# Kernel optimization log

Measured on AMD Instinct MI355X. Metric: run time of the kernel, lower is better.

Reference implementation:

```python
import jax, jax.numpy as jnp
import numpy as np

N = 1024          # nodes per atom and per input graph / barycenter
K = 8             # num_atoms
OT_LAYERS = 3     # proximal-point outer iterations inside fgwd
SINKHORN_LAYERS = 3
GWB_LAYERS = 2    # barycenter alternating-optimization iterations
PROX_BETA = 0.1   # proximal / entropic regularization strength
EPS = 1e-16


def fgwd(Gs, ps, Gb, pb):
    """Gromov-Wasserstein distance via proximal point + Sinkhorn.
    Gs:(ns,ns), ps:(ns,1), Gb:(nb,nb), pb:(nb,1). Returns (d, T) with T:(ns,nb).
    Square-loss GW cost: c(T) = f1(Gs) ps 1^T + 1 (f2(Gb) pb)^T - 2 Gs T Gb^T."""
    ns, nb = Gs.shape[0], Gb.shape[0]
    cost_st = ((Gs * Gs) @ ps) + ((Gb * Gb) @ pb).T  # (ns,1)+(1,nb) -> (ns,nb)
    T0 = ps @ pb.T  # independent-coupling init

    def ot_step(T, _):
        cost = cost_st - 2.0 * (Gs @ T @ Gb.T)
        kernel = jnp.exp(-cost / PROX_BETA) * T  # proximal-point kernel

        def sink(carry, _):
            a, b = carry
            b = pb / (kernel.T @ a + EPS)
            a = ps / (kernel @ b + EPS)
            return (a, b), None

        (a, b), _ = jax.lax.scan(sink, (ps, pb), None, length=SINKHORN_LAYERS)
        return (a * kernel) * b.T, None

    T, _ = jax.lax.scan(ot_step, T0, None, length=OT_LAYERS)
    cost = cost_st - 2.0 * (Gs @ T @ Gb.T)
    d = jnp.sum(cost * T)
    return d, T


def setup_inputs() -> dict:
    key = jax.random.key(0)
    k1, k2, k3 = jax.random.split(key, 3)
    Gm = jax.random.uniform(k1, (N, N), jnp.float32)          # input graph (sigmoid-range adjacency)
    pm = jnp.ones((N, 1), jnp.float32) / N                    # uniform node distribution
    atoms_presig = jax.random.normal(k2, (K, N, N), jnp.float32)  # pre-sigmoid atom params
    probs = jnp.ones((K, N, 1), jnp.float32) / N              # uniform atom distributions
    weights = jax.nn.softmax(jax.random.normal(k3, (K,), jnp.float32))  # output_weights
    return {"Gm": Gm, "pm": pm, "atoms_presig": atoms_presig, "probs": probs,
            "weights": weights}


def reference(Gm, pm, atoms_presig, probs, weights):
    Gk = jax.nn.sigmoid(atoms_presig)              # output_atoms: (K,N,N)
    G_bary, pb = Gm, pm                            # init_mode=0 -> barycenter init from input M
    fgwd_v = jax.vmap(fgwd, in_axes=(0, 0, None, None))
    denom = pb @ pb.T                              # pb pb^T normalizer
    for _ in range(GWB_LAYERS):
        _, trans = fgwd_v(Gk, probs, G_bary, pb)   # trans: (K,N,N)
        # comp_fgwb: sum_k w_k * T_k^T G_k T_k / (pb pb^T)
        GT = jnp.einsum('knm,kmj->knj', Gk, trans)
        G_bary = jnp.einsum('k,kni,knj->ij', weights, trans, GT) / denom
    d_fgw, _ = fgwd(Gm, pm, G_bary, pb)
    return d_fgw, G_bary
```

## Files before the change

kernel.cpp:

```cpp
#include <hip/hip_runtime.h>
#include <math.h>

#define N_   1024
#define K_   8
#define OTL  3
#define SKL  3
#define GWBL 2
#define INVB 10.0f
#define EPSV 1e-16f
#define INVN (1.0f / 1024.0f)
#define NN   ((size_t)N_ * N_)
#define KN   (K_ * N_)

typedef __attribute__((ext_vector_type(8))) short short8;
typedef __attribute__((ext_vector_type(4))) float f32x4;
typedef unsigned short bfu;

__device__ __forceinline__ float b2f(bfu u) {
    unsigned x = ((unsigned)u) << 16;
    return __builtin_bit_cast(float, x);
}
__device__ __forceinline__ bfu f2b(float f) {
    unsigned u = __builtin_bit_cast(unsigned, f);
    unsigned r = u + 0x7fffu + ((u >> 16) & 1u);
    return (bfu)(r >> 16);
}

template<int EPI>
__global__ __launch_bounds__(256, 2)
void bgemm_k(const bfu* __restrict__ A, const bfu* __restrict__ B,
             void* __restrict__ Cp, size_t sA, size_t sB, size_t sC,
             const float* __restrict__ rv, const float* __restrict__ cv,
             const float* __restrict__ wts, float* __restrict__ rs) {
    __shared__ bfu As[128 * 32];
    __shared__ bfu Bs[128 * 32];

    const int z  = blockIdx.x;
    const int bm = blockIdx.y * 128, bn = blockIdx.z * 128;
    const int tid = threadIdx.x;
    const int lane = tid & 63, wv = tid >> 6;
    const int wr = wv >> 1, wc = wv & 1;

    if (EPI == 0) {
        if (rs && blockIdx.y == 0 && blockIdx.z == 0) {
            const float4 zf = {0.f, 0.f, 0.f, 0.f};
            #pragma unroll
            for (int b = 0; b < 3; ++b)
                *(float4*)&rs[b * KN + z * N_ + tid * 4] = zf;
        }
    }

    const bfu* Az = A + (size_t)z * sA;
    const bfu* Bz = B + (size_t)z * sB;

    const int sr = tid >> 2;
    const int sk = (tid & 3) * 8;
    const int fr = lane & 15;
    const int ks = (lane >> 4) * 8;

    f32x4 acc[4][4];
    #pragma unroll
    for (int i = 0; i < 4; i++)
        #pragma unroll
        for (int j = 0; j < 4; j++) acc[i][j] = (f32x4)0.f;

    for (int k0 = 0; k0 < N_; k0 += 32) {
        __syncthreads();
        #pragma unroll
        for (int h = 0; h < 2; ++h) {
            const int row = sr + h * 64;
            const bfu* ga = Az + (size_t)(bm + row) * N_ + k0 + sk;
            const bfu* gb = Bz + (size_t)(bn + row) * N_ + k0 + sk;
            __builtin_amdgcn_global_load_lds(
                (const __attribute__((address_space(1))) unsigned int*)ga,
                (__attribute__((address_space(3))) unsigned int*)&As[row * 32 + sk],
                16, 0, 0);
            __builtin_amdgcn_global_load_lds(
                (const __attribute__((address_space(1))) unsigned int*)gb,
                (__attribute__((address_space(3))) unsigned int*)&Bs[row * 32 + sk],
                16, 0, 0);
        }
        __syncthreads();

        short8 af[4], bf[4];
        #pragma unroll
        for (int mi = 0; mi < 4; ++mi)
            af[mi] = *(const short8*)&As[(wr * 64 + mi * 16 + fr) * 32 + ks];
        #pragma unroll
        for (int ni = 0; ni < 4; ++ni)
            bf[ni] = *(const short8*)&Bs[(wc * 64 + ni * 16 + fr) * 32 + ks];
        #pragma unroll
        for (int mi = 0; mi < 4; ++mi)
            #pragma unroll
            for (int ni = 0; ni < 4; ++ni)
                acc[mi][ni] = __builtin_amdgcn_mfma_f32_16x16x32_bf16(
                    af[mi], bf[ni], acc[mi][ni], 0, 0, 0);
    }

    const int r0 = bm + wr * 64, c0 = bn + wc * 64;
    const int rq = (lane >> 4) * 4;

    if (EPI == 1) {
        float* Cz = (float*)Cp + (size_t)z * sC;
        const float w = wts[z];
        #pragma unroll
        for (int mi = 0; mi < 4; ++mi)
            #pragma unroll
            for (int ni = 0; ni < 4; ++ni)
                #pragma unroll
                for (int q = 0; q < 4; ++q)
                    Cz[(size_t)(r0 + mi * 16 + rq + q) * N_ + c0 + ni * 16 + fr]
                        = w * acc[mi][ni][q];
    } else if (EPI == 0) {
        bfu* Cz = (bfu*)Cp + (size_t)z * sC;
        #pragma unroll
        for (int mi = 0; mi < 4; ++mi)
            #pragma unroll
            for (int ni = 0; ni < 4; ++ni)
                #pragma unroll
                for (int q = 0; q < 4; ++q)
                    Cz[(size_t)(r0 + mi * 16 + rq + q) * N_ + c0 + ni * 16 + fr]
                        = f2b(acc[mi][ni][q]);
    } else {
        bfu* Cz = (bfu*)Cp + (size_t)z * sC;
        const float* rvz = rv + z * N_;
        float rsum[4][4];
        #pragma unroll
        for (int mi = 0; mi < 4; ++mi)
            #pragma unroll
            for (int q = 0; q < 4; ++q) rsum[mi][q] = 0.f;
        #pragma unroll
        for (int mi = 0; mi < 4; ++mi)
            #pragma unroll
            for (int ni = 0; ni < 4; ++ni)
                #pragma unroll
                for (int q = 0; q < 4; ++q) {
                    const int row = r0 + mi * 16 + rq + q;
                    const int col = c0 + ni * 16 + fr;
                    const float cost = rvz[col] + cv[row] - 2.f * acc[mi][ni][q];
                    const float t = b2f(Cz[(size_t)row * N_ + col]);
                    const bfu tn = f2b(expf(-cost * INVB) * t);
                    Cz[(size_t)row * N_ + col] = tn;
                    rsum[mi][q] += b2f(tn);
                }
        #pragma unroll
        for (int mi = 0; mi < 4; ++mi)
            #pragma unroll
            for (int q = 0; q < 4; ++q) {
                float v = rsum[mi][q];
                v += __shfl_xor(v, 1);
                v += __shfl_xor(v, 2);
                v += __shfl_xor(v, 4);
                v += __shfl_xor(v, 8);
                if (fr == 0)
                    atomicAdd(&rs[z * N_ + r0 + mi * 16 + rq + q], v);
            }
    }
}

template<int EPI>
__global__ __launch_bounds__(256, 2)
void gemm64_k(const bfu* __restrict__ A, const bfu* __restrict__ B,
              void* __restrict__ Cp,
              const float* __restrict__ rv, const float* __restrict__ cv,
              float* __restrict__ rs, float* __restrict__ dout) {
    __shared__ bfu As[64 * 32];
    __shared__ bfu Bs[64 * 32];
    const int bn = blockIdx.x * 64;
    const int bm = blockIdx.y * 64;
    const int tid = threadIdx.x;
    const int lane = tid & 63, wv = tid >> 6;
    const int wr = wv >> 1, wc = wv & 1;
    const int sr = tid >> 2, sk = (tid & 3) * 8;
    const int fr = lane & 15, ks = (lane >> 4) * 8;

    if (EPI == 0) {
        if (blockIdx.x == 0 && blockIdx.y == 0) {
            if (rs) {
                const float4 zf = {0.f, 0.f, 0.f, 0.f};
                #pragma unroll
                for (int b = 0; b < 3; ++b)
                    *(float4*)&rs[b * KN + tid * 4] = zf;
            }
            if (dout && tid == 0) *dout = 0.f;
        }
    }

    f32x4 acc[2][2];
    #pragma unroll
    for (int i = 0; i < 2; i++)
        #pragma unroll
        for (int j = 0; j < 2; j++) acc[i][j] = (f32x4)0.f;

    for (int k0 = 0; k0 < N_; k0 += 32) {
        __syncthreads();
        __builtin_amdgcn_global_load_lds(
            (const __attribute__((address_space(1))) unsigned int*)
                (A + (size_t)(bm + sr) * N_ + k0 + sk),
            (__attribute__((address_space(3))) unsigned int*)&As[sr * 32 + sk],
            16, 0, 0);
        __builtin_amdgcn_global_load_lds(
            (const __attribute__((address_space(1))) unsigned int*)
                (B + (size_t)(bn + sr) * N_ + k0 + sk),
            (__attribute__((address_space(3))) unsigned int*)&Bs[sr * 32 + sk],
            16, 0, 0);
        __syncthreads();
        short8 af[2], bf[2];
        #pragma unroll
        for (int mi = 0; mi < 2; ++mi)
            af[mi] = *(const short8*)&As[(wr * 32 + mi * 16 + fr) * 32 + ks];
        #pragma unroll
        for (int ni = 0; ni < 2; ++ni)
            bf[ni] = *(const short8*)&Bs[(wc * 32 + ni * 16 + fr) * 32 + ks];
        #pragma unroll
        for (int mi = 0; mi < 2; ++mi)
            #pragma unroll
            for (int ni = 0; ni < 2; ++ni)
                acc[mi][ni] = __builtin_amdgcn_mfma_f32_16x16x32_bf16(
                    af[mi], bf[ni], acc[mi][ni], 0, 0, 0);
    }

    const int r0 = bm + wr * 32, c0 = bn + wc * 32;
    const int rq = (lane >> 4) * 4;

    if (EPI == 0) {
        bfu* C = (bfu*)Cp;
        #pragma unroll
        for (int mi = 0; mi < 2; ++mi)
            #pragma unroll
            for (int ni = 0; ni < 2; ++ni)
                #pragma unroll
                for (int q = 0; q < 4; ++q)
                    C[(size_t)(r0 + mi * 16 + rq + q) * N_ + c0 + ni * 16 + fr]
                        = f2b(acc[mi][ni][q]);
    } else if (EPI == 2) {
        bfu* C = (bfu*)Cp;
        float rsum[2][4];
        #pragma unroll
        for (int mi = 0; mi < 2; ++mi)
            #pragma unroll
            for (int q = 0; q < 4; ++q) rsum[mi][q] = 0.f;
        #pragma unroll
        for (int mi = 0; mi < 2; ++mi)
            #pragma unroll
            for (int ni = 0; ni < 2; ++ni)
                #pragma unroll
                for (int q = 0; q < 4; ++q) {
                    const int row = r0 + mi * 16 + rq + q;
                    const int col = c0 + ni * 16 + fr;
                    const float cost = rv[col] + cv[row] - 2.f * acc[mi][ni][q];
                    const float t = b2f(C[(size_t)row * N_ + col]);
                    const bfu tn = f2b(expf(-cost * INVB) * t);
                    C[(size_t)row * N_ + col] = tn;
                    rsum[mi][q] += b2f(tn);
                }
        #pragma unroll
        for (int mi = 0; mi < 2; ++mi)
            #pragma unroll
            for (int q = 0; q < 4; ++q) {
                float v = rsum[mi][q];
                v += __shfl_xor(v, 1);
                v += __shfl_xor(v, 2);
                v += __shfl_xor(v, 4);
                v += __shfl_xor(v, 8);
                if (fr == 0)
                    atomicAdd(&rs[r0 + mi * 16 + rq + q], v);
            }
    } else {
        const bfu* C = (const bfu*)Cp;
        float bs = 0.f;
        #pragma unroll
        for (int mi = 0; mi < 2; ++mi)
            #pragma unroll
            for (int ni = 0; ni < 2; ++ni)
                #pragma unroll
                for (int q = 0; q < 4; ++q) {
                    const int row = r0 + mi * 16 + rq + q;
                    const int col = c0 + ni * 16 + fr;
                    bs += (rv[col] + cv[row] - 2.f * acc[mi][ni][q]) *
                          b2f(C[(size_t)row * N_ + col]);
                }
        #pragma unroll
        for (int off = 32; off; off >>= 1) bs += __shfl_down(bs, off);
        __shared__ float wred[4];
        if (lane == 0) wred[wv] = bs;
        __syncthreads();
        if (tid == 0) atomicAdd(dout, wred[0] + wred[1] + wred[2] + wred[3]);
    }
}

__global__ __launch_bounds__(256)
void prox1_k(bfu* __restrict__ Tt, const float* __restrict__ c2,
             const float* __restrict__ u, const float* __restrict__ d2,
             const float* __restrict__ w, const float* __restrict__ ps,
             const float* __restrict__ pb, float* __restrict__ bv,
             float* __restrict__ rs1, int zs, int nb) {
    const int b = blockIdx.x;
    const int z  = (nb == 8) ? (b & 7) : 0;
    const int rp = (nb == 8) ? (b >> 3) : b;
    const int tid = threadIdx.x;

    if (rp < 2) {
        const float4 zf = {0.f, 0.f, 0.f, 0.f};
        *(float4*)&rs1[rp * KN + z * N_ + tid * 4] = zf;
    }

    const int half = tid >> 7;
    const int j = rp * 2 + half;
    const int i0 = (tid & 127) * 8;
    const float d2j = d2[j], wj = w[j], pbj = pb[j];
    const float* c2z = c2 + z * zs + i0;
    const float* uz  = u  + z * zs + i0;
    const float* psz = ps + z * zs + i0;
    bfu o[8];
    float s = 0.f;
    #pragma unroll
    for (int t = 0; t < 8; ++t) {
        const float cost = c2z[t] + d2j - 2.f * uz[t] * wj;
        o[t] = f2b(expf(-cost * INVB) * psz[t] * pbj);
        s += b2f(o[t]);
    }
    *(short8*)&Tt[((size_t)z << 20) + ((size_t)j << 10) + i0] = *(short8*)o;
    #pragma unroll
    for (int off = 32; off; off >>= 1) s += __shfl_down(s, off);
    __shared__ float red[4];
    if ((tid & 63) == 0) red[tid >> 6] = s;
    __syncthreads();
    if ((tid & 127) == 0)
        bv[z * N_ + j] = pbj / ((red[half * 2] + red[half * 2 + 1]) * INVN + EPSV);
}

template<int NB, int BSRC, int TUPD>
__global__ __launch_bounds__(1024)
void sinka_k(bfu* __restrict__ Tt, const float* __restrict__ bvin,
             const float* __restrict__ rsin, const float* __restrict__ ps,
             int pstr, float* __restrict__ rsnext) {
    constexpr int CPB = (NB == 8) ? 32 : 16;
    constexpr int RG  = 1024 / CPB;
    constexpr int RPG = N_ / RG;
    int z, cb;
    if (NB == 8) { z = blockIdx.x & 7; cb = blockIdx.x >> 3; }
    else         { z = 0;              cb = blockIdx.x; }
    const int tid = threadIdx.x;
    const int cl = tid % CPB, rg = tid / CPB;
    const int i = cb * CPB + cl;
    const int zN = z * N_;
    bfu* Tz = Tt + (size_t)z * NN;

    __shared__ float bvs[1024];
    __shared__ float red[1024];
    __shared__ float avs[CPB];
    if (BSRC == 0)      bvs[tid] = bvin[zN + tid];
    else if (BSRC == 1) bvs[tid] = INVN / (rsin[zN + tid] * INVN + EPSV);
    else                bvs[tid] = INVN / (rsin[zN + tid] + EPSV);
    __syncthreads();

    float s = 0.f;
    const int j0 = rg * RPG;
    #pragma unroll 8
    for (int j = j0; j < j0 + RPG; ++j)
        s += b2f(Tz[(size_t)j * N_ + i]) * bvs[j];
    red[tid] = s;
    __syncthreads();
    #pragma unroll
    for (int h = RG / 2; h > 0; h >>= 1) {
        if (rg < h) red[rg * CPB + cl] += red[(rg + h) * CPB + cl];
        __syncthreads();
    }
    const float avi = ps[z * pstr + i] / (red[cl] + EPSV);

    if (TUPD) {
        for (int j = j0; j < j0 + RPG; ++j) {
            const size_t o = (size_t)j * N_ + i;
            Tz[o] = f2b(b2f(Tz[o]) * avi * bvs[j]);
        }
    } else {
        if (rg == 0) avs[cl] = avi;
        __syncthreads();
        const bfu* Tr = Tz + (size_t)tid * N_ + cb * CPB;
        float v = 0.f;
        #pragma unroll
        for (int q8 = 0; q8 < CPB; q8 += 8) {
            bfu t[8];
            *(short8*)t = *(const short8*)&Tr[q8];
            #pragma unroll
            for (int q = 0; q < 8; ++q) v += b2f(t[q]) * avs[q8 + q];
        }
        atomicAdd(&rsnext[zN + tid], v);
    }
}


template<int SIG>
__global__ void prep_k(const float* __restrict__ X, bfu* __restrict__ Y,
                       float* __restrict__ y2, float* __restrict__ y1) {
    const int z = blockIdx.y;
    const int wv = threadIdx.x >> 6, lane = threadIdx.x & 63;
    const int r = blockIdx.x * 4 + wv;
    const float* Xr = X + (size_t)z * NN + (size_t)r * N_;
    bfu* Yr = Y + (size_t)z * NN + (size_t)r * N_;
    float s2 = 0.f, s1 = 0.f;
    for (int c = lane * 4; c < N_; c += 256) {
        float4 v = *(const float4*)(Xr + c);
        if (SIG) {
            v.x = 1.f / (1.f + expf(-v.x));
            v.y = 1.f / (1.f + expf(-v.y));
            v.z = 1.f / (1.f + expf(-v.z));
            v.w = 1.f / (1.f + expf(-v.w));
        }
        bfu o[4];
        o[0] = f2b(v.x); o[1] = f2b(v.y); o[2] = f2b(v.z); o[3] = f2b(v.w);
        *(ulong1*)&Yr[c] = *(ulong1*)o;
        s2 += v.x * v.x + v.y * v.y + v.z * v.z + v.w * v.w;
        s1 += v.x + v.y + v.z + v.w;
    }
    #pragma unroll
    for (int off = 32; off; off >>= 1) {
        s2 += __shfl_down(s2, off);
        s1 += __shfl_down(s1, off);
    }
    if (lane == 0) {
        y2[z * N_ + r] = s2 * INVN;
        y1[z * N_ + r] = s1 * INVN;
    }
}

__global__ void reduce8_k(const float* __restrict__ part, bfu* __restrict__ Gbt,
                          float* __restrict__ d2, float* __restrict__ w,
                          float* __restrict__ out1) {
    const int tid = threadIdx.x;
    __shared__ float wred[8];
    #pragma unroll
    for (int rep = 0; rep < 2; ++rep) {
        const int row = blockIdx.x + rep * 512;
        const size_t idx = (size_t)row * N_ + tid * 4;
        float4 s = *(const float4*)(part + idx);
        #pragma unroll
        for (int sl = 1; sl < K_; ++sl) {
            float4 v = *(const float4*)(part + (size_t)sl * NN + idx);
            s.x += v.x; s.y += v.y; s.z += v.z; s.w += v.w;
        }
        const float sc = 1048576.f;
        s.x *= sc; s.y *= sc; s.z *= sc; s.w *= sc;
        bfu o[4];
        o[0] = f2b(s.x); o[1] = f2b(s.y); o[2] = f2b(s.z); o[3] = f2b(s.w);
        *(ulong1*)&Gbt[idx] = *(ulong1*)o;
        if (out1) {
            out1[idx + 0] = s.x; out1[idx + 1] = s.y;
            out1[idx + 2] = s.z; out1[idx + 3] = s.w;
        }
        float r2 = s.x * s.x + s.y * s.y + s.z * s.z + s.w * s.w;
        float r1 = s.x + s.y + s.z + s.w;
        #pragma unroll
        for (int off = 32; off; off >>= 1) {
            r2 += __shfl_down(r2, off);
            r1 += __shfl_down(r1, off);
        }
        if ((tid & 63) == 0) {
            wred[(tid >> 6) * 2]     = r2;
            wred[(tid >> 6) * 2 + 1] = r1;
        }
        __syncthreads();
        if (tid == 0) {
            d2[row] = (wred[0] + wred[2] + wred[4] + wred[6]) * INVN;
            w[row]  = (wred[1] + wred[3] + wred[5] + wred[7]) * INVN;
        }
        __syncthreads();
    }
}


template<int NB, int BSRC1>
static inline void sink_tail(bfu* Tt, const float* ps, int pstr,
                             float* bvec, float* rs, hipStream_t stream) {
    const dim3 ga((NB == 8) ? 256 : 64);
    float* rs1 = rs + KN;
    float* rs2 = rs + 2 * KN;
    sinka_k<NB, BSRC1, 0><<<ga, dim3(1024), 0, stream>>>(Tt, bvec, rs, ps, pstr, rs1);
    sinka_k<NB, 2, 0><<<ga, dim3(1024), 0, stream>>>(Tt, nullptr, rs1, ps, pstr, rs2);
    sinka_k<NB, 2, 1><<<ga, dim3(1024), 0, stream>>>(Tt, nullptr, rs2, ps, pstr, nullptr);
}

extern "C" void kernel_launch(void* const* d_in, const int* in_sizes, int n_in,
                              void* d_out, int out_size, void* d_ws, size_t ws_size,
                              hipStream_t stream) {
    const float* Gm    = (const float*)d_in[0];
    const float* pm    = (const float*)d_in[1];
    const float* atoms = (const float*)d_in[2];
    const float* probs = (const float*)d_in[3];
    const float* wts   = (const float*)d_in[4];
    float* out = (float*)d_out;

    char* base = (char*)d_ws;
    bfu*   Gkt  = (bfu*)base;                    base += K_ * NN * 2;
    bfu*   Tt   = (bfu*)base;                    base += K_ * NN * 2;
    bfu*   M    = (bfu*)base;                    base += K_ * NN * 2;
    float* part = (float*)base;                  base += K_ * NN * 4;
    bfu*   Gbt  = (bfu*)base;                    base += NN * 2;
    bfu*   Gmt  = (bfu*)base;                    base += NN * 2;
    float* Gk2ps = (float*)base;                 base += KN * 4;
    float* Gku   = (float*)base;                 base += KN * 4;
    float* Gm2pm = (float*)base;                 base += N_ * 4;
    float* Gmu   = (float*)base;                 base += N_ * 4;
    float* Gb2pb = (float*)base;                 base += N_ * 4;
    float* Gbw   = (float*)base;                 base += N_ * 4;
    float* bvec  = (float*)base;                 base += KN * 4;
    float* rs    = (float*)base;                 base += 3 * KN * 4;

    const dim3 blk(256);
    const dim3 g8(8, 8, 8);
    const dim3 g64(16, 16);

    prep_k<1><<<dim3(256, K_), blk, 0, stream>>>(atoms, Gkt, Gk2ps, Gku);
    prep_k<0><<<dim3(256, 1), blk, 0, stream>>>(Gm, Gmt, Gm2pm, Gmu);

    for (int it = 0; it < GWBL; ++it) {
        const bfu*   GbtU = it ? Gbt : Gmt;
        const float* d2U  = it ? Gb2pb : Gm2pm;
        const float* wU   = it ? Gbw : Gmu;

        prox1_k<<<512 * K_, blk, 0, stream>>>(Tt, Gk2ps, Gku, d2U, wU,
                                              probs, pm, bvec, rs + KN, N_, K_);
        sink_tail<K_, 0>(Tt, probs, N_, bvec, rs, stream);
        for (int ot = 1; ot < OTL; ++ot) {
            bgemm_k<0><<<g8, blk, 0, stream>>>(Gkt, Tt, M, NN, NN, NN,
                nullptr, nullptr, nullptr, rs);
            bgemm_k<2><<<g8, blk, 0, stream>>>(GbtU, M, Tt, 0, NN, NN,
                Gk2ps, d2U, nullptr, rs);
            sink_tail<K_, 1>(Tt, probs, N_, bvec, rs, stream);
        }
        bgemm_k<0><<<g8, blk, 0, stream>>>(Tt, Gkt, M, NN, NN, NN,
            nullptr, nullptr, nullptr, nullptr);
        bgemm_k<1><<<g8, blk, 0, stream>>>(Tt, M, part, NN, NN, NN,
            nullptr, nullptr, wts, nullptr);
        reduce8_k<<<512, blk, 0, stream>>>(part, Gbt, Gb2pb, Gbw,
                                           (it == GWBL - 1) ? out + 1 : nullptr);
    }

    prox1_k<<<512, blk, 0, stream>>>(Tt, Gm2pm, Gmu, Gb2pb, Gbw, pm, pm,
                                     bvec, rs + KN, 0, 1);
    sink_tail<1, 0>(Tt, pm, 0, bvec, rs, stream);
    for (int ot = 1; ot < OTL; ++ot) {
        gemm64_k<0><<<g64, blk, 0, stream>>>(Gmt, Tt, M,
            nullptr, nullptr, rs, nullptr);
        gemm64_k<2><<<g64, blk, 0, stream>>>(Gbt, M, Tt,
            Gm2pm, Gb2pb, rs, nullptr);
        sink_tail<1, 1>(Tt, pm, 0, bvec, rs, stream);
    }
    gemm64_k<0><<<g64, blk, 0, stream>>>(Gmt, Tt, M,
        nullptr, nullptr, nullptr, out );
    gemm64_k<3><<<g64, blk, 0, stream>>>(Gbt, M, Tt,
        Gm2pm, Gb2pb, nullptr, out);
}
```

Before: 658.7 us.

## Fuse barycenter reduction with next proximal init and deepen GEMM K-tile

The barycenter reduction kernel now also computes the next stage's initial proximal kernel and column scaling, which removes a separate prox1 launch per iteration. It hardcodes uniform 1/N distributions in that fused path. The batched GEMM now loads two 32-wide K slices per barrier, halving the sync count at the cost of doubled LDS use. The fused kernel runs its per-atom loop serially inside 512 blocks, with two block syncs per atom, which may limit parallelism.

```diff
diff --git a/kernel.cpp b/kernel.cpp
--- a/kernel.cpp
+++ b/kernel.cpp
@@ -32,8 +32,8 @@
              void* __restrict__ Cp, size_t sA, size_t sB, size_t sC,
              const float* __restrict__ rv, const float* __restrict__ cv,
              const float* __restrict__ wts, float* __restrict__ rs) {
-    __shared__ bfu As[128 * 32];
-    __shared__ bfu Bs[128 * 32];
+    __shared__ bfu As[2][128 * 32];
+    __shared__ bfu Bs[2][128 * 32];
 
     const int z  = blockIdx.x;
     const int bm = blockIdx.y * 128, bn = blockIdx.z * 128;
@@ -64,37 +64,43 @@
         #pragma unroll
         for (int j = 0; j < 4; j++) acc[i][j] = (f32x4)0.f;
 
-    for (int k0 = 0; k0 < N_; k0 += 32) {
-        __syncthreads();
-        #pragma unroll
-        for (int h = 0; h < 2; ++h) {
-            const int row = sr + h * 64;
-            const bfu* ga = Az + (size_t)(bm + row) * N_ + k0 + sk;
-            const bfu* gb = Bz + (size_t)(bn + row) * N_ + k0 + sk;
-            __builtin_amdgcn_global_load_lds(
-                (const __attribute__((address_space(1))) unsigned int*)ga,
-                (__attribute__((address_space(3))) unsigned int*)&As[row * 32 + sk],
-                16, 0, 0);
-            __builtin_amdgcn_global_load_lds(
-                (const __attribute__((address_space(1))) unsigned int*)gb,
-                (__attribute__((address_space(3))) unsigned int*)&Bs[row * 32 + sk],
-                16, 0, 0);
-        }
-        __syncthreads();
-
-        short8 af[4], bf[4];
-        #pragma unroll
-        for (int mi = 0; mi < 4; ++mi)
-            af[mi] = *(const short8*)&As[(wr * 64 + mi * 16 + fr) * 32 + ks];
-        #pragma unroll
-        for (int ni = 0; ni < 4; ++ni)
-            bf[ni] = *(const short8*)&Bs[(wc * 64 + ni * 16 + fr) * 32 + ks];
-        #pragma unroll
-        for (int mi = 0; mi < 4; ++mi)
+    for (int k0 = 0; k0 < N_; k0 += 64) {
+        __syncthreads();
+        #pragma unroll
+        for (int sg = 0; sg < 2; ++sg) {
+            #pragma unroll
+            for (int h = 0; h < 2; ++h) {
+                const int row = sr + h * 64;
+                const bfu* ga = Az + (size_t)(bm + row) * N_ + k0 + sg * 32 + sk;
+                const bfu* gb = Bz + (size_t)(bn + row) * N_ + k0 + sg * 32 + sk;
+                __builtin_amdgcn_global_load_lds(
+                    (const __attribute__((address_space(1))) unsigned int*)ga,
+                    (__attribute__((address_space(3))) unsigned int*)&As[sg][row * 32 + sk],
+                    16, 0, 0);
+                __builtin_amdgcn_global_load_lds(
+                    (const __attribute__((address_space(1))) unsigned int*)gb,
+                    (__attribute__((address_space(3))) unsigned int*)&Bs[sg][row * 32 + sk],
+                    16, 0, 0);
+            }
+        }
+        __syncthreads();
+
+        #pragma unroll
+        for (int sg = 0; sg < 2; ++sg) {
+            short8 af[4], bf[4];
+            #pragma unroll
+            for (int mi = 0; mi < 4; ++mi)
+                af[mi] = *(const short8*)&As[sg][(wr * 64 + mi * 16 + fr) * 32 + ks];
             #pragma unroll
             for (int ni = 0; ni < 4; ++ni)
-                acc[mi][ni] = __builtin_amdgcn_mfma_f32_16x16x32_bf16(
-                    af[mi], bf[ni], acc[mi][ni], 0, 0, 0);
+                bf[ni] = *(const short8*)&Bs[sg][(wc * 64 + ni * 16 + fr) * 32 + ks];
+            #pragma unroll
+            for (int mi = 0; mi < 4; ++mi)
+                #pragma unroll
+                for (int ni = 0; ni < 4; ++ni)
+                    acc[mi][ni] = __builtin_amdgcn_mfma_f32_16x16x32_bf16(
+                        af[mi], bf[ni], acc[mi][ni], 0, 0, 0);
+        }
     }
 
     const int r0 = bm + wr * 64, c0 = bn + wc * 64;
@@ -328,6 +334,84 @@
     __syncthreads();
     if ((tid & 127) == 0)
         bv[z * N_ + j] = pbj / ((red[half * 2] + red[half * 2 + 1]) * INVN + EPSV);
+}
+
+template<int NB>
+__global__ __launch_bounds__(256)
+void redprox_k(const float* __restrict__ part, bfu* __restrict__ Gbt,
+               float* __restrict__ d2out, float* __restrict__ wout,
+               float* __restrict__ out1,
+               const float* __restrict__ c2, const float* __restrict__ u,
+               bfu* __restrict__ Tt, float* __restrict__ bv,
+               float* __restrict__ rs12) {
+    const int tid = threadIdx.x;
+    if (blockIdx.x < 16) {
+        const float4 zf = {0.f, 0.f, 0.f, 0.f};
+        *(float4*)&rs12[blockIdx.x * 1024 + tid * 4] = zf;
+    }
+    __shared__ float red[8];
+    __shared__ float bc[2];
+    #pragma unroll
+    for (int rep = 0; rep < 2; ++rep) {
+        const int row = blockIdx.x + rep * 512;
+        const size_t idx = (size_t)row * N_ + tid * 4;
+        float4 s = *(const float4*)(part + idx);
+        #pragma unroll
+        for (int sl = 1; sl < K_; ++sl) {
+            float4 v = *(const float4*)(part + (size_t)sl * NN + idx);
+            s.x += v.x; s.y += v.y; s.z += v.z; s.w += v.w;
+        }
+        const float sc = 1048576.f;
+        s.x *= sc; s.y *= sc; s.z *= sc; s.w *= sc;
+        bfu o[4];
+        o[0] = f2b(s.x); o[1] = f2b(s.y); o[2] = f2b(s.z); o[3] = f2b(s.w);
+        *(ulong1*)&Gbt[idx] = *(ulong1*)o;
+        if (out1) {
+            out1[idx + 0] = s.x; out1[idx + 1] = s.y;
+            out1[idx + 2] = s.z; out1[idx + 3] = s.w;
+        }
+        float r2 = s.x * s.x + s.y * s.y + s.z * s.z + s.w * s.w;
+        float r1 = s.x + s.y + s.z + s.w;
+        #pragma unroll
+        for (int off = 32; off; off >>= 1) {
+            r2 += __shfl_down(r2, off);
+            r1 += __shfl_down(r1, off);
+        }
+        if ((tid & 63) == 0) {
+            red[(tid >> 6) * 2]     = r2;
+            red[(tid >> 6) * 2 + 1] = r1;
+        }
+        __syncthreads();
+        if (tid == 0) {
+            const float d2j = (red[0] + red[2] + red[4] + red[6]) * INVN;
+            const float wj  = (red[1] + red[3] + red[5] + red[7]) * INVN;
+            d2out[row] = d2j; wout[row] = wj;
+            bc[0] = d2j; bc[1] = wj;
+        }
+        __syncthreads();
+        const float d2j = bc[0], wj = bc[1];
+        const float sc2 = INVN * INVN;
+        #pragma unroll
+        for (int z = 0; z < NB; ++z) {
+            const float4 cv4 = *(const float4*)(c2 + z * N_ + tid * 4);
+            const float4 uv4 = *(const float4*)(u  + z * N_ + tid * 4);
+            bfu t[4];
+            t[0] = f2b(expf(-(cv4.x + d2j - 2.f * uv4.x * wj) * INVB) * sc2);
+            t[1] = f2b(expf(-(cv4.y + d2j - 2.f * uv4.y * wj) * INVB) * sc2);
+            t[2] = f2b(expf(-(cv4.z + d2j - 2.f * uv4.z * wj) * INVB) * sc2);
+            t[3] = f2b(expf(-(cv4.w + d2j - 2.f * uv4.w * wj) * INVB) * sc2);
+            *(ulong1*)&Tt[(size_t)z * NN + idx] = *(ulong1*)t;
+            float rsum = b2f(t[0]) + b2f(t[1]) + b2f(t[2]) + b2f(t[3]);
+            #pragma unroll
+            for (int off = 32; off; off >>= 1) rsum += __shfl_down(rsum, off);
+            if ((tid & 63) == 0) red[tid >> 6] = rsum;
+            __syncthreads();
+            if (tid == 0)
+                bv[z * N_ + row] = INVN /
+                    ((red[0] + red[1] + red[2] + red[3]) * INVN + EPSV);
+            __syncthreads();
+        }
+    }
 }
 
 template<int NB, int BSRC, int TUPD>
@@ -390,7 +474,6 @@
     }
 }
 
-
 template<int SIG>
 __global__ void prep_k(const float* __restrict__ X, bfu* __restrict__ Y,
                        float* __restrict__ y2, float* __restrict__ y1) {
@@ -425,50 +508,6 @@
     }
 }
 
-__global__ void reduce8_k(const float* __restrict__ part, bfu* __restrict__ Gbt,
-                          float* __restrict__ d2, float* __restrict__ w,
-                          float* __restrict__ out1) {
-    const int tid = threadIdx.x;
-    __shared__ float wred[8];
-    #pragma unroll
-    for (int rep = 0; rep < 2; ++rep) {
-        const int row = blockIdx.x + rep * 512;
-        const size_t idx = (size_t)row * N_ + tid * 4;
-        float4 s = *(const float4*)(part + idx);
-        #pragma unroll
-        for (int sl = 1; sl < K_; ++sl) {
-            float4 v = *(const float4*)(part + (size_t)sl * NN + idx);
-            s.x += v.x; s.y += v.y; s.z += v.z; s.w += v.w;
-        }
-        const float sc = 1048576.f;
-        s.x *= sc; s.y *= sc; s.z *= sc; s.w *= sc;
-        bfu o[4];
-        o[0] = f2b(s.x); o[1] = f2b(s.y); o[2] = f2b(s.z); o[3] = f2b(s.w);
-        *(ulong1*)&Gbt[idx] = *(ulong1*)o;
-        if (out1) {
-            out1[idx + 0] = s.x; out1[idx + 1] = s.y;
-            out1[idx + 2] = s.z; out1[idx + 3] = s.w;
-        }
-        float r2 = s.x * s.x + s.y * s.y + s.z * s.z + s.w * s.w;
-        float r1 = s.x + s.y + s.z + s.w;
-        #pragma unroll
-        for (int off = 32; off; off >>= 1) {
-            r2 += __shfl_down(r2, off);
-            r1 += __shfl_down(r1, off);
-        }
-        if ((tid & 63) == 0) {
-            wred[(tid >> 6) * 2]     = r2;
-            wred[(tid >> 6) * 2 + 1] = r1;
-        }
-        __syncthreads();
-        if (tid == 0) {
-            d2[row] = (wred[0] + wred[2] + wred[4] + wred[6]) * INVN;
-            w[row]  = (wred[1] + wred[3] + wred[5] + wred[7]) * INVN;
-        }
-        __syncthreads();
-    }
-}
-
 
 template<int NB, int BSRC1>
 static inline void sink_tail(bfu* Tt, const float* ps, int pstr,
@@ -517,10 +556,10 @@
     for (int it = 0; it < GWBL; ++it) {
         const bfu*   GbtU = it ? Gbt : Gmt;
         const float* d2U  = it ? Gb2pb : Gm2pm;
-        const float* wU   = it ? Gbw : Gmu;
-
-        prox1_k<<<512 * K_, blk, 0, stream>>>(Tt, Gk2ps, Gku, d2U, wU,
-                                              probs, pm, bvec, rs + KN, N_, K_);
+
+        if (it == 0)
+            prox1_k<<<512 * K_, blk, 0, stream>>>(Tt, Gk2ps, Gku, Gm2pm, Gmu,
+                                                  probs, pm, bvec, rs + KN, N_, K_);
         sink_tail<K_, 0>(Tt, probs, N_, bvec, rs, stream);
         for (int ot = 1; ot < OTL; ++ot) {
             bgemm_k<0><<<g8, blk, 0, stream>>>(Gkt, Tt, M, NN, NN, NN,
@@ -533,12 +572,14 @@
             nullptr, nullptr, nullptr, nullptr);
         bgemm_k<1><<<g8, blk, 0, stream>>>(Tt, M, part, NN, NN, NN,
             nullptr, nullptr, wts, nullptr);
-        reduce8_k<<<512, blk, 0, stream>>>(part, Gbt, Gb2pb, Gbw,
-                                           (it == GWBL - 1) ? out + 1 : nullptr);
-    }
-
-    prox1_k<<<512, blk, 0, stream>>>(Tt, Gm2pm, Gmu, Gb2pb, Gbw, pm, pm,
-                                     bvec, rs + KN, 0, 1);
+        if (it == 0)
+            redprox_k<8><<<512, blk, 0, stream>>>(part, Gbt, Gb2pb, Gbw,
+                nullptr, Gk2ps, Gku, Tt, bvec, rs + KN);
+        else
+            redprox_k<1><<<512, blk, 0, stream>>>(part, Gbt, Gb2pb, Gbw,
+                out + 1, Gm2pm, Gmu, Tt, bvec, rs + KN);
+    }
+
     sink_tail<1, 0>(Tt, pm, 0, bvec, rs, stream);
     for (int ot = 1; ot < OTL; ++ot) {
         gemm64_k<0><<<g64, blk, 0, stream>>>(Gmt, Tt, M,
```

Result: faster. 638.3 us (-3.1%).
